# Kernel optimization log

Hardware: AMD Instinct MI355X
Metric: run time of the kernel (lower is better)

## Reference

```python
import jax, jax.numpy as jnp
import numpy as np

H = 512   # hidden_size == mm_dim
C = 8     # chunks
R = 8     # rank
S = H // C  # chunk size = 64
OUT = 512 # output_dim of linear_merge
EPS = 1e-12

def _linear(x, w, b):
    # torch nn.Linear convention: w [out, in]
    return x @ w.T + b

def setup_inputs() -> dict:
    key = jax.random.key(0)
    ks = jax.random.split(key, 24)
    B, Lq, Lk, D = 8, 160, 160, 512
    s = 0.02
    inp = {
        'v': jax.random.normal(ks[0], (B, Lk, D), jnp.float32),
        'k': jax.random.normal(ks[1], (B, Lk, D), jnp.float32),
        'q': jax.random.normal(ks[2], (B, Lq, D), jnp.float32),
        # input projections
        'w_v': jax.random.normal(ks[3], (H, D)) * s, 'b_v': jnp.zeros((H,)),
        'w_k': jax.random.normal(ks[4], (H, D)) * s, 'b_k': jnp.zeros((H,)),
        'w_q': jax.random.normal(ks[5], (H, D)) * s, 'b_q': jnp.zeros((H,)),
        # Block: linear0 (applied to key), linear1 (applied to query)
        'w0': jax.random.normal(ks[6], (H, H)) * s, 'b0': jnp.zeros((H,)),
        'w1': jax.random.normal(ks[7], (H, H)) * s, 'b1': jnp.zeros((H,)),
        # per-chunk merge linears, stacked: [C, S*R, S]
        'wm0': jax.random.normal(ks[8], (C, S * R, S)) * s, 'bm0': jnp.zeros((C, S * R)),
        'wm1': jax.random.normal(ks[9], (C, S * R, S)) * s, 'bm1': jnp.zeros((C, S * R)),
        # Block linear_out: mm_dim -> 1
        'w_bo': jax.random.normal(ks[10], (1, H)) * s, 'b_bo': jnp.zeros((1,)),
        # linear_merge: hidden -> output_dim
        'w_m': jax.random.normal(ks[11], (OUT, H)) * s, 'b_m': jnp.zeros((OUT,)),
    }
    return inp

def _block_scores(kx, qx, w0, b0, w1, b1, wm0, bm0, wm1, bm1, w_bo, b_bo):
    # kx: [B,Lk,H] (block arg 0 = key), qx: [B,Lq,H] (block arg 1 = query)
    x0 = _linear(kx, w0, b0)                      # [B,Lk,H]
    x1 = _linear(qx, w1, b1)                      # [B,Lq,H]
    B_, Lk = x0.shape[0], x0.shape[1]
    Lq = x1.shape[1]
    x0c = x0.reshape(B_, Lk, C, S)
    x1c = x1.reshape(B_, Lq, C, S)
    # per-chunk merge projections to rank*size
    y0 = jnp.einsum('bkcs,cts->bkct', x0c, wm0) + bm0  # [B,Lk,C,R*S]
    y1 = jnp.einsum('bqcs,cts->bqct', x1c, wm1) + bm1  # [B,Lq,C,R*S]
    y0 = y0.reshape(B_, Lk, C, R, S)
    y1 = y1.reshape(B_, Lq, C, R, S)
    # elementwise product summed over rank, pairwise over (q,k)
    z = jnp.einsum('bqcrs,bkcrs->bqkcs', y1, y0)  # [B,Lq,Lk,C,S]
    # signed sqrt (power norm) then per-chunk L2 normalize
    z = jnp.sqrt(jax.nn.relu(z)) - jnp.sqrt(jax.nn.relu(-z))
    z = z / jnp.maximum(jnp.linalg.norm(z, axis=-1, keepdims=True), EPS)
    z = z.reshape(B_, Lq, Lk, C * S)
    return _linear(z, w_bo, b_bo).squeeze(-1)     # [B,Lq,Lk]

def reference(v, k, q, w_v, b_v, w_k, b_k, w_q, b_q, w0, b0, w1, b1,
              wm0, bm0, wm1, bm1, w_bo, b_bo, w_m, b_m):
    vv = _linear(v, w_v, b_v)   # [B,Lk,H]
    kk = _linear(k, w_k, b_k)   # [B,Lk,H]
    qq = _linear(q, w_q, b_q)   # [B,Lq,H]
    scores = _block_scores(kk, qq, w0, b0, w1, b1, wm0, bm0, wm1, bm1, w_bo, b_bo)
    att = jax.nn.softmax(scores, axis=-1)          # dropout = identity (eval)
    atted = jnp.einsum('bqk,bkh->bqh', att, vv)    # [B,Lq,H]
    B_ = atted.shape[0]
    # faithful to torch: transpose(1,2).contiguous().view(B,-1,H)
    atted = jnp.swapaxes(atted, 1, 2).reshape(B_, -1, H)
    out = _linear(atted, w_m, b_m)                 # [B,Lq,OUT]
    return jnp.squeeze(out)
```

## Files before the change

kernel.cpp:

```cpp
#include <hip/hip_runtime.h>
#include <hip/hip_bf16.h>

#define B_  8
#define LQ  160
#define LK  160

typedef __attribute__((ext_vector_type(8))) short bf16x8;
typedef __attribute__((ext_vector_type(4))) float f32x4;

static __device__ __forceinline__ ushort f2bf(float f) {
    union { float f; unsigned u; } v; v.f = f;
    const unsigned r = (v.u + 0x7FFF + ((v.u >> 16) & 1)) >> 16;
    return (ushort)r;
}

struct CastArgs { const float4* src[6]; ushort4* dst[6]; int n[6]; };

__global__ __launch_bounds__(256) void cast_bf16k(CastArgs a)
{
    const int seg = blockIdx.y;
    const int i = blockIdx.x * 256 + threadIdx.x;
    if (i < a.n[seg]) {
        const float4 v = a.src[seg][i];
        ushort4 u;
        u.x = f2bf(v.x); u.y = f2bf(v.y); u.z = f2bf(v.z); u.w = f2bf(v.w);
        a.dst[seg][i] = u;
    }
}

struct MfmaOps { const ushort* A[2]; const ushort* W[2]; const float* Bi[2]; void* C[2]; };

template <int OUTBF>
__global__ __launch_bounds__(256) void mfma_g(MfmaOps ops)
{
    const int op = blockIdx.z;
    const ushort* __restrict__ A  = ops.A[op];
    const ushort* __restrict__ W  = ops.W[op];
    const float*  __restrict__ Bi = ops.Bi[op];

    const int m0 = blockIdx.y << 6;
    const int n0 = blockIdx.x << 6;
    const int tid  = threadIdx.x;
    const int wave = tid >> 6;
    const int lane = tid & 63;
    const int l16  = lane & 15;
    const int kg   = (lane >> 4) << 3;

    const ushort* Ap = A + (long)(m0 + (wave << 4) + l16) * 512 + kg;
    const ushort* Wp = W + (long)(n0 + l16) * 512 + kg;

    f32x4 acc[4] = {{0.f,0.f,0.f,0.f},{0.f,0.f,0.f,0.f},
                    {0.f,0.f,0.f,0.f},{0.f,0.f,0.f,0.f}};
    for (int k0 = 0; k0 < 512; k0 += 32) {
        const bf16x8 a = *(const bf16x8*)(Ap + k0);
#pragma unroll
        for (int nf = 0; nf < 4; nf++) {
            const bf16x8 b = *(const bf16x8*)(Wp + nf * (16 * 512) + k0);
            acc[nf] = __builtin_amdgcn_mfma_f32_16x16x32_bf16(a, b, acc[nf], 0, 0, 0);
        }
    }

    const int mrow = m0 + (wave << 4) + ((lane >> 4) << 2);
#pragma unroll
    for (int nf = 0; nf < 4; nf++) {
        const int n = n0 + (nf << 4) + l16;
        const float bias = Bi[n];
        if (OUTBF) {
            ushort* C = (ushort*)ops.C[op];
#pragma unroll
            for (int r = 0; r < 4; r++)
                C[(long)(mrow + r) * 512 + n] = f2bf(acc[nf][r] + bias);
        } else {
            float* C = (float*)ops.C[op];
#pragma unroll
            for (int r = 0; r < 4; r++)
                C[(long)(mrow + r) * 512 + n] = acc[nf][r] + bias;
        }
    }
}

struct GOps {
    const float* A[3];
    const float* W[3];
    const float* Bi[3];
    float*       C[3];
};

__global__ __launch_bounds__(256) void gemm_f(GOps ops, int K)
{
    const int op = blockIdx.z;
    const float* __restrict__ A  = ops.A[op];
    const float* __restrict__ W  = ops.W[op];
    const float* __restrict__ Bi = ops.Bi[op];
    float* __restrict__       C  = ops.C[op];

    const int m0 = blockIdx.y << 6;
    const int n0 = blockIdx.x << 6;
    const int tid = threadIdx.x;
    const int tm  = tid >> 4;
    const int tn  = tid & 15;
    const int lr  = tid >> 2;
    const int lk4 = (tid & 3) << 2;

    __shared__ float As[16][64];
    __shared__ float Ws[16][64];

    float acc[4][4];
#pragma unroll
    for (int i = 0; i < 4; i++)
#pragma unroll
        for (int j = 0; j < 4; j++) acc[i][j] = 0.f;

    const float* Arow = A + (long)(m0 + lr) * 512 + lk4;
    const float* Wrow = W + (long)(n0 + lr) * K + lk4;
    float4 av = *(const float4*)(Arow);
    float4 wv = *(const float4*)(Wrow);

    for (int k0 = 0; k0 < K; k0 += 16) {
        __syncthreads();
        As[lk4 + 0][lr] = av.x; As[lk4 + 1][lr] = av.y;
        As[lk4 + 2][lr] = av.z; As[lk4 + 3][lr] = av.w;
        Ws[lk4 + 0][lr] = wv.x; Ws[lk4 + 1][lr] = wv.y;
        Ws[lk4 + 2][lr] = wv.z; Ws[lk4 + 3][lr] = wv.w;
        __syncthreads();
        if (k0 + 16 < K) {
            av = *(const float4*)(Arow + k0 + 16);
            wv = *(const float4*)(Wrow + k0 + 16);
        }
#pragma unroll
        for (int kk = 0; kk < 16; kk++) {
            const float4 a4 = *(const float4*)(&As[kk][tm << 2]);
            const float4 b4 = *(const float4*)(&Ws[kk][tn << 2]);
            const float aa[4] = {a4.x, a4.y, a4.z, a4.w};
            const float bb[4] = {b4.x, b4.y, b4.z, b4.w};
#pragma unroll
            for (int i = 0; i < 4; i++)
#pragma unroll
                for (int j = 0; j < 4; j++)
                    acc[i][j] = fmaf(aa[i], bb[j], acc[i][j]);
        }
    }

    const float4 bv = *(const float4*)(Bi + n0 + (tn << 2));
    const float bArr[4] = {bv.x, bv.y, bv.z, bv.w};

#pragma unroll
    for (int i = 0; i < 4; i++) {
        float4 vo;
        vo.x = acc[i][0] + bArr[0]; vo.y = acc[i][1] + bArr[1];
        vo.z = acc[i][2] + bArr[2]; vo.w = acc[i][3] + bArr[3];
        *(float4*)(C + (long)(m0 + (tm << 2) + i) * 512 + n0 + (tn << 2)) = vo;
    }
}

__global__ __launch_bounds__(256) void y_proj(
    const float* __restrict__ x0, const float* __restrict__ wm0, const float* __restrict__ bm0,
    const float* __restrict__ x1, const float* __restrict__ wm1, const float* __restrict__ bm1,
    float* __restrict__ y0t, float* __restrict__ y1p)
{
    const int z   = blockIdx.z;
    const bool is1 = z >= 8;
    const int c   = is1 ? z - 8 : z;
    const float* A  = (is1 ? x1 : x0) + (c << 6);
    const float* W  = (is1 ? wm1 : wm0) + c * 32768;
    const float* Bi = (is1 ? bm1 : bm0) + (c << 9);

    const int m0 = blockIdx.y << 6;
    const int s0 = blockIdx.x << 3;
    const int tid = threadIdx.x;
    const int tm  = tid >> 4;
    const int tn  = tid & 15;
    const int lr  = tid >> 2;
    const int lk4 = (tid & 3) << 2;

    __shared__ float As[16][64];
    __shared__ float Ws[16][64];
    __shared__ float outT[4096];

    float acc[4][4];
#pragma unroll
    for (int i = 0; i < 4; i++)
#pragma unroll
        for (int j = 0; j < 4; j++) acc[i][j] = 0.f;

    const int wrow = ((lr & 7) << 6) + s0 + (lr >> 3);
    const float* Arow = A + (long)(m0 + lr) * 512 + lk4;
    const float* Wrow = W + (long)wrow * 64 + lk4;
    float4 av = *(const float4*)(Arow);
    float4 wv = *(const float4*)(Wrow);

    for (int k0 = 0; k0 < 64; k0 += 16) {
        __syncthreads();
        As[lk4 + 0][lr] = av.x; As[lk4 + 1][lr] = av.y;
        As[lk4 + 2][lr] = av.z; As[lk4 + 3][lr] = av.w;
        Ws[lk4 + 0][lr] = wv.x; Ws[lk4 + 1][lr] = wv.y;
        Ws[lk4 + 2][lr] = wv.z; Ws[lk4 + 3][lr] = wv.w;
        __syncthreads();
        if (k0 + 16 < 64) {
            av = *(const float4*)(Arow + k0 + 16);
            wv = *(const float4*)(Wrow + k0 + 16);
        }
#pragma unroll
        for (int kk = 0; kk < 16; kk++) {
            const float4 a4 = *(const float4*)(&As[kk][tm << 2]);
            const float4 b4 = *(const float4*)(&Ws[kk][tn << 2]);
            const float aa[4] = {a4.x, a4.y, a4.z, a4.w};
            const float bb[4] = {b4.x, b4.y, b4.z, b4.w};
#pragma unroll
            for (int i = 0; i < 4; i++)
#pragma unroll
                for (int j = 0; j < 4; j++)
                    acc[i][j] = fmaf(aa[i], bb[j], acc[i][j]);
        }
    }

    float bArr[4];
#pragma unroll
    for (int j = 0; j < 4; j++) {
        const int ln = (tn << 2) + j;
        bArr[j] = Bi[((ln & 7) << 6) + s0 + (ln >> 3)];
    }
    __syncthreads();
    if (is1) {
#pragma unroll
        for (int i = 0; i < 4; i++) {
            const int m8 = (tm << 2) + i;
#pragma unroll
            for (int j = 0; j < 4; j++) {
                const int ln = (tn << 2) + j;
                outT[(m8 << 6) + ((ln >> 3) << 3) + (ln & 7)] = acc[i][j] + bArr[j];
            }
        }
        __syncthreads();
#pragma unroll
        for (int p = 0; p < 4; p++) {
            const int idx = tid + (p << 8);
            const int m8  = idx >> 4;
            const int f4  = idx & 15;
            *(float4*)(y1p + (long)(m0 + m8) * 4096 + (c << 9) + (s0 << 3) + (f4 << 2))
                = *(const float4*)&outT[idx << 2];
        }
    } else {
#pragma unroll
        for (int i = 0; i < 4; i++) {
            const int k8 = (tm << 2) + i;
#pragma unroll
            for (int j = 0; j < 4; j++) {
                const int ln = (tn << 2) + j;
                outT[((ln >> 3) << 9) + (k8 << 3) + (ln & 7)] = acc[i][j] + bArr[j];
            }
        }
        __syncthreads();
#pragma unroll
        for (int p = 0; p < 4; p++) {
            const int s8  = (p << 1) + (tid >> 7);
            const int u4  = tid & 127;
            const int k8  = u4 >> 1;
            const int r   = (u4 & 1) << 2;
            const int m   = m0 + k8;
            const int bidx = m / 160;
            const int kmod = m - bidx * 160;
            const int s   = s0 + s8;
            float4* dst = (float4*)(y0t +
                (((long)(bidx * 8 + c) * 64 + s) * 160 + kmod) * 8 + r);
            *dst = *(const float4*)&outT[(s8 << 9) + (u4 << 2)];
        }
    }
}

__global__ __launch_bounds__(192) void score_partial(
    const float* __restrict__ y1p, const float* __restrict__ y0t,
    const float* __restrict__ wbo, float* __restrict__ scores_p)
{
    const int id = blockIdx.x;
    const int c  = id & 7;
    const int j  = id >> 3;
    const int b  = j / 40;
    const int q0 = (j - b * 40) << 2;
    const int k  = threadIdx.x;
    const int kc = k < LK ? k : (LK - 1);

    const float* wb = wbo + (c << 6);
    const float* y1r0 = y1p + (long)(b * LQ + q0) * 4096 + (c << 9);
    const float* y1r1 = y1r0 + 4096;
    const float* y1r2 = y1r0 + 8192;
    const float* y1r3 = y1r0 + 12288;
    const float* ybc = y0t + (((long)(b * 8 + c) * 64) * 160 + kc) * 8;

    float num[4] = {0.f, 0.f, 0.f, 0.f};
    float den[4] = {0.f, 0.f, 0.f, 0.f};

    float4 a0 = *(const float4*)(ybc);
    float4 a1 = *(const float4*)(ybc + 4);
#pragma unroll 2
    for (int s = 0; s < 64; s++) {
        const float a[8] = {a0.x, a0.y, a0.z, a0.w, a1.x, a1.y, a1.z, a1.w};
        const int sn = (s + 1) & 63;
        a0 = *(const float4*)(ybc + (long)sn * 1280);
        a1 = *(const float4*)(ybc + (long)sn * 1280 + 4);
        const float w = wb[s];
        const int o = s << 3;
        {
            float zv = a[0] * y1r0[o];
            zv = fmaf(a[1], y1r0[o+1], zv); zv = fmaf(a[2], y1r0[o+2], zv);
            zv = fmaf(a[3], y1r0[o+3], zv); zv = fmaf(a[4], y1r0[o+4], zv);
            zv = fmaf(a[5], y1r0[o+5], zv); zv = fmaf(a[6], y1r0[o+6], zv);
            zv = fmaf(a[7], y1r0[o+7], zv);
            const float az = fabsf(zv);
            num[0] = fmaf(copysignf(__builtin_amdgcn_sqrtf(az), zv), w, num[0]);
            den[0] += az;
        }
        {
            float zv = a[0] * y1r1[o];
            zv = fmaf(a[1], y1r1[o+1], zv); zv = fmaf(a[2], y1r1[o+2], zv);
            zv = fmaf(a[3], y1r1[o+3], zv); zv = fmaf(a[4], y1r1[o+4], zv);
            zv = fmaf(a[5], y1r1[o+5], zv); zv = fmaf(a[6], y1r1[o+6], zv);
            zv = fmaf(a[7], y1r1[o+7], zv);
            const float az = fabsf(zv);
            num[1] = fmaf(copysignf(__builtin_amdgcn_sqrtf(az), zv), w, num[1]);
            den[1] += az;
        }
        {
            float zv = a[0] * y1r2[o];
            zv = fmaf(a[1], y1r2[o+1], zv); zv = fmaf(a[2], y1r2[o+2], zv);
            zv = fmaf(a[3], y1r2[o+3], zv); zv = fmaf(a[4], y1r2[o+4], zv);
            zv = fmaf(a[5], y1r2[o+5], zv); zv = fmaf(a[6], y1r2[o+6], zv);
            zv = fmaf(a[7], y1r2[o+7], zv);
            const float az = fabsf(zv);
            num[2] = fmaf(copysignf(__builtin_amdgcn_sqrtf(az), zv), w, num[2]);
            den[2] += az;
        }
        {
            float zv = a[0] * y1r3[o];
            zv = fmaf(a[1], y1r3[o+1], zv); zv = fmaf(a[2], y1r3[o+2], zv);
            zv = fmaf(a[3], y1r3[o+3], zv); zv = fmaf(a[4], y1r3[o+4], zv);
            zv = fmaf(a[5], y1r3[o+5], zv); zv = fmaf(a[6], y1r3[o+6], zv);
            zv = fmaf(a[7], y1r3[o+7], zv);
            const float az = fabsf(zv);
            num[3] = fmaf(copysignf(__builtin_amdgcn_sqrtf(az), zv), w, num[3]);
            den[3] += az;
        }
    }
    if (k < LK) {
#pragma unroll
        for (int q = 0; q < 4; q++)
            scores_p[(((long)(b * LQ + q0 + q)) * 8 + c) * 160 + k] =
                num[q] / fmaxf(__builtin_amdgcn_sqrtf(den[q]), 1e-12f);
    }
}

__global__ __launch_bounds__(256) void softmax_attv(
    const float* __restrict__ scores_p, const float* __restrict__ vv,
    float* __restrict__ attedT)
{
    const int b  = blockIdx.y;
    const int q0 = blockIdx.x << 2;
    const int tid = threadIdx.x;

    __shared__ float scs[4][160];
    __shared__ float invd[4];

    for (int t = tid; t < 640; t += 256) {
        const int q = t / 160;
        const int k = t - q * 160;
        const float* sp = scores_p + ((long)(b * LQ + q0 + q)) * 1280 + k;
        float s = 0.f;
#pragma unroll
        for (int c = 0; c < 8; c++) s += sp[c * 160];
        scs[q][k] = s;
    }
    __syncthreads();

    const int w    = tid >> 6;
    const int lane = tid & 63;
    {
        const int q = w;
        float m = -1e30f;
        for (int kk = lane; kk < LK; kk += 64) m = fmaxf(m, scs[q][kk]);
#pragma unroll
        for (int off = 32; off; off >>= 1) m = fmaxf(m, __shfl_xor(m, off, 64));
        float sum = 0.f;
        for (int kk = lane; kk < LK; kk += 64) {
            const float e = __expf(scs[q][kk] - m);
            scs[q][kk] = e;
            sum += e;
        }
#pragma unroll
        for (int off = 32; off; off >>= 1) sum += __shfl_xor(sum, off, 64);
        if (lane == 0) invd[q] = 1.f / sum;
    }
    __syncthreads();

    float acc[2][4] = {{0.f,0.f,0.f,0.f},{0.f,0.f,0.f,0.f}};
    const float* vb = vv + (long)b * (LK * 512);
    for (int kk = 0; kk < LK; kk++) {
        const float* vr = vb + kk * 512;
        const float p0 = scs[0][kk], p1 = scs[1][kk];
        const float p2 = scs[2][kk], p3 = scs[3][kk];
        const float v0 = vr[tid], v1 = vr[tid + 256];
        acc[0][0] = fmaf(p0, v0, acc[0][0]); acc[0][1] = fmaf(p1, v0, acc[0][1]);
        acc[0][2] = fmaf(p2, v0, acc[0][2]); acc[0][3] = fmaf(p3, v0, acc[0][3]);
        acc[1][0] = fmaf(p0, v1, acc[1][0]); acc[1][1] = fmaf(p1, v1, acc[1][1]);
        acc[1][2] = fmaf(p2, v1, acc[1][2]); acc[1][3] = fmaf(p3, v1, acc[1][3]);
    }
#pragma unroll
    for (int j = 0; j < 2; j++) {
        const int h = tid + (j << 8);
#pragma unroll
        for (int q = 0; q < 4; q++)
            attedT[((long)b * 512 + h) * 160 + q0 + q] = acc[j][q] * invd[q];
    }
}

extern "C" void kernel_launch(void* const* d_in, const int* in_sizes, int n_in,
                              void* d_out, int out_size, void* d_ws, size_t ws_size,
                              hipStream_t stream) {
    const float* v    = (const float*)d_in[0];
    const float* kin  = (const float*)d_in[1];
    const float* q    = (const float*)d_in[2];
    const float* w_v  = (const float*)d_in[3];
    const float* b_v  = (const float*)d_in[4];
    const float* w_k  = (const float*)d_in[5];
    const float* b_k  = (const float*)d_in[6];
    const float* w_q  = (const float*)d_in[7];
    const float* b_q  = (const float*)d_in[8];
    const float* w0   = (const float*)d_in[9];
    const float* b0   = (const float*)d_in[10];
    const float* w1   = (const float*)d_in[11];
    const float* b1   = (const float*)d_in[12];
    const float* wm0  = (const float*)d_in[13];
    const float* bm0  = (const float*)d_in[14];
    const float* wm1  = (const float*)d_in[15];
    const float* bm1  = (const float*)d_in[16];
    const float* w_bo = (const float*)d_in[17];
    (void)d_in[18];
    const float* w_m  = (const float*)d_in[19];
    const float* b_m  = (const float*)d_in[20];

    float* ws       = (float*)d_ws;
    float* vv       = ws;
    ushort* kbf     = (ushort*)(ws + 655360);
    ushort* qbf     = kbf + 655360;
    ushort* kkbf    = (ushort*)(ws + 1310720);
    ushort* qqbf    = kkbf + 655360;
    float* x0       = ws + 1966080;
    float* x1       = ws + 2621440;
    float* y1p      = ws + 3276800;
    float* y0t      = ws + 8519680;
    float* attedT   = ws + 13762560;
    ushort* wkbf    = (ushort*)(ws + 14417920);
    ushort* wqbf    = wkbf + 262144;
    ushort* w0bf    = wkbf + 524288;
    ushort* w1bf    = wkbf + 786432;
    float* scores_p = ws + 655360;

    CastArgs ca;
    ca.src[0] = (const float4*)kin; ca.dst[0] = (ushort4*)kbf;  ca.n[0] = 163840;
    ca.src[1] = (const float4*)q;   ca.dst[1] = (ushort4*)qbf;  ca.n[1] = 163840;
    ca.src[2] = (const float4*)w_k; ca.dst[2] = (ushort4*)wkbf; ca.n[2] = 65536;
    ca.src[3] = (const float4*)w_q; ca.dst[3] = (ushort4*)wqbf; ca.n[3] = 65536;
    ca.src[4] = (const float4*)w0;  ca.dst[4] = (ushort4*)w0bf; ca.n[4] = 65536;
    ca.src[5] = (const float4*)w1;  ca.dst[5] = (ushort4*)w1bf; ca.n[5] = 65536;
    hipLaunchKernelGGL(cast_bf16k, dim3(640, 6), dim3(256), 0, stream, ca);

    GOps oV;
    oV.A[0] = v; oV.W[0] = w_v; oV.Bi[0] = b_v; oV.C[0] = vv;
    oV.A[1] = oV.A[2] = nullptr; oV.W[1] = oV.W[2] = nullptr;
    oV.Bi[1] = oV.Bi[2] = nullptr; oV.C[1] = oV.C[2] = nullptr;
    hipLaunchKernelGGL(gemm_f, dim3(8, 20, 1), dim3(256), 0, stream, oV, 512);

    MfmaOps mA;
    mA.A[0] = kbf; mA.W[0] = wkbf; mA.Bi[0] = b_k; mA.C[0] = kkbf;
    mA.A[1] = qbf; mA.W[1] = wqbf; mA.Bi[1] = b_q; mA.C[1] = qqbf;
    hipLaunchKernelGGL((mfma_g<1>), dim3(8, 20, 2), dim3(256), 0, stream, mA);

    MfmaOps mB;
    mB.A[0] = kkbf; mB.W[0] = w0bf; mB.Bi[0] = b0; mB.C[0] = x0;
    mB.A[1] = qqbf; mB.W[1] = w1bf; mB.Bi[1] = b1; mB.C[1] = x1;
    hipLaunchKernelGGL((mfma_g<0>), dim3(8, 20, 2), dim3(256), 0, stream, mB);

    hipLaunchKernelGGL(y_proj, dim3(8, 20, 16), dim3(256), 0, stream,
                       x0, wm0, bm0, x1, wm1, bm1, y0t, y1p);

    hipLaunchKernelGGL(score_partial, dim3(2560), dim3(192), 0, stream,
                       y1p, y0t, w_bo, scores_p);

    hipLaunchKernelGGL(softmax_attv, dim3(40, 8), dim3(256), 0, stream,
                       scores_p, vv, attedT);

    GOps oF;
    oF.A[0] = attedT; oF.W[0] = w_m; oF.Bi[0] = b_m; oF.C[0] = (float*)d_out;
    oF.A[1] = oF.A[2] = nullptr; oF.W[1] = oF.W[2] = nullptr;
    oF.Bi[1] = oF.Bi[2] = nullptr; oF.C[1] = oF.C[2] = nullptr;
    hipLaunchKernelGGL(gemm_f, dim3(8, 20, 1), dim3(256), 0, stream, oF, 512);
}
```

Before: 298.3 us.

## Compute pairwise rank-sum scores with bf16 MFMA and a shared y layout

y_proj now writes both y0 and y1 as bf16 in one common transposed layout [b,c,s,row,r]. The scalar FP32 score_partial kernel is replaced by score_mfma, which uses 16x16x32 bf16 MFMA to compute the rank-8 dot products for 16 queries by 32 keys per wave. Only 8 of the 32 K slots are filled and the rest are zeros. The aim is to cut the FP32 FMA work and halve the memory traffic of the y tensors, at the cost of bf16 rounding before the signed sqrt and a largely idle MFMA K dimension.

```diff
diff --git a/kernel.cpp b/kernel.cpp
--- a/kernel.cpp
+++ b/kernel.cpp
@@ -156,7 +156,7 @@
 __global__ __launch_bounds__(256) void y_proj(
     const float* __restrict__ x0, const float* __restrict__ wm0, const float* __restrict__ bm0,
     const float* __restrict__ x1, const float* __restrict__ wm1, const float* __restrict__ bm1,
-    float* __restrict__ y0t, float* __restrict__ y1p)
+    ushort* __restrict__ y0f, ushort* __restrict__ y1f)
 {
     const int z   = blockIdx.z;
     const bool is1 = z >= 8;
@@ -164,6 +164,7 @@
     const float* A  = (is1 ? x1 : x0) + (c << 6);
     const float* W  = (is1 ? wm1 : wm0) + c * 32768;
     const float* Bi = (is1 ? bm1 : bm0) + (c << 9);
+    ushort* __restrict__ dstT = is1 ? y1f : y0f;
 
     const int m0 = blockIdx.y << 6;
     const int s0 = blockIdx.x << 3;
@@ -221,131 +222,91 @@
         bArr[j] = Bi[((ln & 7) << 6) + s0 + (ln >> 3)];
     }
     __syncthreads();
-    if (is1) {
-#pragma unroll
-        for (int i = 0; i < 4; i++) {
-            const int m8 = (tm << 2) + i;
-#pragma unroll
-            for (int j = 0; j < 4; j++) {
-                const int ln = (tn << 2) + j;
-                outT[(m8 << 6) + ((ln >> 3) << 3) + (ln & 7)] = acc[i][j] + bArr[j];
-            }
-        }
-        __syncthreads();
-#pragma unroll
-        for (int p = 0; p < 4; p++) {
-            const int idx = tid + (p << 8);
-            const int m8  = idx >> 4;
-            const int f4  = idx & 15;
-            *(float4*)(y1p + (long)(m0 + m8) * 4096 + (c << 9) + (s0 << 3) + (f4 << 2))
-                = *(const float4*)&outT[idx << 2];
-        }
-    } else {
-#pragma unroll
-        for (int i = 0; i < 4; i++) {
-            const int k8 = (tm << 2) + i;
-#pragma unroll
-            for (int j = 0; j < 4; j++) {
-                const int ln = (tn << 2) + j;
-                outT[((ln >> 3) << 9) + (k8 << 3) + (ln & 7)] = acc[i][j] + bArr[j];
-            }
-        }
-        __syncthreads();
-#pragma unroll
-        for (int p = 0; p < 4; p++) {
-            const int s8  = (p << 1) + (tid >> 7);
-            const int u4  = tid & 127;
-            const int k8  = u4 >> 1;
-            const int r   = (u4 & 1) << 2;
-            const int m   = m0 + k8;
-            const int bidx = m / 160;
-            const int kmod = m - bidx * 160;
-            const int s   = s0 + s8;
-            float4* dst = (float4*)(y0t +
-                (((long)(bidx * 8 + c) * 64 + s) * 160 + kmod) * 8 + r);
-            *dst = *(const float4*)&outT[(s8 << 9) + (u4 << 2)];
-        }
-    }
-}
-
-__global__ __launch_bounds__(192) void score_partial(
-    const float* __restrict__ y1p, const float* __restrict__ y0t,
+#pragma unroll
+    for (int i = 0; i < 4; i++) {
+        const int r8 = (tm << 2) + i;
+#pragma unroll
+        for (int j = 0; j < 4; j++) {
+            const int ln = (tn << 2) + j;
+            outT[((ln >> 3) << 9) + (r8 << 3) + (ln & 7)] = acc[i][j] + bArr[j];
+        }
+    }
+    __syncthreads();
+#pragma unroll
+    for (int p = 0; p < 4; p++) {
+        const int s8  = (p << 1) + (tid >> 7);
+        const int u4  = tid & 127;
+        const int r8  = u4 >> 1;
+        const int r   = (u4 & 1) << 2;
+        const int m   = m0 + r8;
+        const int bidx = m / 160;
+        const int rmod = m - bidx * 160;
+        const int s   = s0 + s8;
+        const float* src = &outT[(s8 << 9) + (u4 << 2)];
+        ushort4 u;
+        u.x = f2bf(src[0]); u.y = f2bf(src[1]);
+        u.z = f2bf(src[2]); u.w = f2bf(src[3]);
+        *(ushort4*)(dstT + (((long)(bidx * 8 + c) * 64 + s) * 160 + rmod) * 8 + r) = u;
+    }
+}
+
+__global__ __launch_bounds__(320) void score_mfma(
+    const ushort* __restrict__ y1f, const ushort* __restrict__ y0f,
     const float* __restrict__ wbo, float* __restrict__ scores_p)
 {
-    const int id = blockIdx.x;
-    const int c  = id & 7;
-    const int j  = id >> 3;
-    const int b  = j / 40;
-    const int q0 = (j - b * 40) << 2;
-    const int k  = threadIdx.x;
-    const int kc = k < LK ? k : (LK - 1);
-
-    const float* wb = wbo + (c << 6);
-    const float* y1r0 = y1p + (long)(b * LQ + q0) * 4096 + (c << 9);
-    const float* y1r1 = y1r0 + 4096;
-    const float* y1r2 = y1r0 + 8192;
-    const float* y1r3 = y1r0 + 12288;
-    const float* ybc = y0t + (((long)(b * 8 + c) * 64) * 160 + kc) * 8;
-
-    float num[4] = {0.f, 0.f, 0.f, 0.f};
-    float den[4] = {0.f, 0.f, 0.f, 0.f};
-
-    float4 a0 = *(const float4*)(ybc);
-    float4 a1 = *(const float4*)(ybc + 4);
-#pragma unroll 2
+    const int bid = blockIdx.x;
+    const int c  = bid & 7;
+    const int b  = (bid >> 3) & 7;
+    const int qt = bid >> 6;
+    const int tid  = threadIdx.x;
+    const int wave = tid >> 6;
+    const int lane = tid & 63;
+    const int l16  = lane & 15;
+    const int g    = lane >> 4;
+    const int q0   = qt << 4;
+    const int k0   = wave << 5;
+
+    const long cbase = (long)(b * 8 + c) * 81920;
+    const float wreg = wbo[(c << 6) + lane];
+
+    f32x4 num0 = {0.f,0.f,0.f,0.f}, den0 = {0.f,0.f,0.f,0.f};
+    f32x4 num1 = {0.f,0.f,0.f,0.f}, den1 = {0.f,0.f,0.f,0.f};
+    const f32x4 zc = {0.f,0.f,0.f,0.f};
+    const bf16x8 zv8 = {0,0,0,0,0,0,0,0};
+
     for (int s = 0; s < 64; s++) {
-        const float a[8] = {a0.x, a0.y, a0.z, a0.w, a1.x, a1.y, a1.z, a1.w};
-        const int sn = (s + 1) & 63;
-        a0 = *(const float4*)(ybc + (long)sn * 1280);
-        a1 = *(const float4*)(ybc + (long)sn * 1280 + 4);
-        const float w = wb[s];
-        const int o = s << 3;
-        {
-            float zv = a[0] * y1r0[o];
-            zv = fmaf(a[1], y1r0[o+1], zv); zv = fmaf(a[2], y1r0[o+2], zv);
-            zv = fmaf(a[3], y1r0[o+3], zv); zv = fmaf(a[4], y1r0[o+4], zv);
-            zv = fmaf(a[5], y1r0[o+5], zv); zv = fmaf(a[6], y1r0[o+6], zv);
-            zv = fmaf(a[7], y1r0[o+7], zv);
-            const float az = fabsf(zv);
-            num[0] = fmaf(copysignf(__builtin_amdgcn_sqrtf(az), zv), w, num[0]);
-            den[0] += az;
-        }
-        {
-            float zv = a[0] * y1r1[o];
-            zv = fmaf(a[1], y1r1[o+1], zv); zv = fmaf(a[2], y1r1[o+2], zv);
-            zv = fmaf(a[3], y1r1[o+3], zv); zv = fmaf(a[4], y1r1[o+4], zv);
-            zv = fmaf(a[5], y1r1[o+5], zv); zv = fmaf(a[6], y1r1[o+6], zv);
-            zv = fmaf(a[7], y1r1[o+7], zv);
-            const float az = fabsf(zv);
-            num[1] = fmaf(copysignf(__builtin_amdgcn_sqrtf(az), zv), w, num[1]);
-            den[1] += az;
-        }
-        {
-            float zv = a[0] * y1r2[o];
-            zv = fmaf(a[1], y1r2[o+1], zv); zv = fmaf(a[2], y1r2[o+2], zv);
-            zv = fmaf(a[3], y1r2[o+3], zv); zv = fmaf(a[4], y1r2[o+4], zv);
-            zv = fmaf(a[5], y1r2[o+5], zv); zv = fmaf(a[6], y1r2[o+6], zv);
-            zv = fmaf(a[7], y1r2[o+7], zv);
-            const float az = fabsf(zv);
-            num[2] = fmaf(copysignf(__builtin_amdgcn_sqrtf(az), zv), w, num[2]);
-            den[2] += az;
-        }
-        {
-            float zv = a[0] * y1r3[o];
-            zv = fmaf(a[1], y1r3[o+1], zv); zv = fmaf(a[2], y1r3[o+2], zv);
-            zv = fmaf(a[3], y1r3[o+3], zv); zv = fmaf(a[4], y1r3[o+4], zv);
-            zv = fmaf(a[5], y1r3[o+5], zv); zv = fmaf(a[6], y1r3[o+6], zv);
-            zv = fmaf(a[7], y1r3[o+7], zv);
-            const float az = fabsf(zv);
-            num[3] = fmaf(copysignf(__builtin_amdgcn_sqrtf(az), zv), w, num[3]);
-            den[3] += az;
-        }
-    }
-    if (k < LK) {
-#pragma unroll
-        for (int q = 0; q < 4; q++)
-            scores_p[(((long)(b * LQ + q0 + q)) * 8 + c) * 160 + k] =
-                num[q] / fmaxf(__builtin_amdgcn_sqrtf(den[q]), 1e-12f);
+        const float w = __shfl(wreg, s, 64);
+        const ushort* row = y1f + cbase + (long)s * 1280;
+        const ushort* row0 = y0f + cbase + (long)s * 1280;
+        bf16x8 a = zv8, b0 = zv8, b1 = zv8;
+        if (g == 0) {
+            a  = *(const bf16x8*)(row  + (q0 + l16) * 8);
+            b0 = *(const bf16x8*)(row0 + (k0 + l16) * 8);
+            b1 = *(const bf16x8*)(row0 + (k0 + 16 + l16) * 8);
+        }
+        const f32x4 z0 = __builtin_amdgcn_mfma_f32_16x16x32_bf16(a, b0, zc, 0, 0, 0);
+        const f32x4 z1 = __builtin_amdgcn_mfma_f32_16x16x32_bf16(a, b1, zc, 0, 0, 0);
+#pragma unroll
+        for (int r4 = 0; r4 < 4; r4++) {
+            const float zz0 = z0[r4];
+            const float az0 = fabsf(zz0);
+            num0[r4] = fmaf(copysignf(__builtin_amdgcn_sqrtf(az0), zz0), w, num0[r4]);
+            den0[r4] += az0;
+            const float zz1 = z1[r4];
+            const float az1 = fabsf(zz1);
+            num1[r4] = fmaf(copysignf(__builtin_amdgcn_sqrtf(az1), zz1), w, num1[r4]);
+            den1[r4] += az1;
+        }
+    }
+
+#pragma unroll
+    for (int r4 = 0; r4 < 4; r4++) {
+        const int q = q0 + (g << 2) + r4;
+        const long rowb = ((long)(b * LQ + q) * 8 + c) * 160;
+        scores_p[rowb + k0 + l16] =
+            num0[r4] / fmaxf(__builtin_amdgcn_sqrtf(den0[r4]), 1e-12f);
+        scores_p[rowb + k0 + 16 + l16] =
+            num1[r4] / fmaxf(__builtin_amdgcn_sqrtf(den1[r4]), 1e-12f);
     }
 }
 
@@ -445,14 +406,14 @@
     ushort* qqbf    = kkbf + 655360;
     float* x0       = ws + 1966080;
     float* x1       = ws + 2621440;
-    float* y1p      = ws + 3276800;
-    float* y0t      = ws + 8519680;
-    float* attedT   = ws + 13762560;
-    ushort* wkbf    = (ushort*)(ws + 14417920);
+    ushort* y1f     = (ushort*)(ws + 3276800);
+    ushort* y0f     = (ushort*)(ws + 5898240);
+    float* attedT   = ws + 8519680;
+    float* scores_p = ws + 9175040;
+    ushort* wkbf    = (ushort*)(ws + 10813440);
     ushort* wqbf    = wkbf + 262144;
     ushort* w0bf    = wkbf + 524288;
     ushort* w1bf    = wkbf + 786432;
-    float* scores_p = ws + 655360;
 
     CastArgs ca;
     ca.src[0] = (const float4*)kin; ca.dst[0] = (ushort4*)kbf;  ca.n[0] = 163840;
@@ -480,10 +441,10 @@
     hipLaunchKernelGGL((mfma_g<0>), dim3(8, 20, 2), dim3(256), 0, stream, mB);
 
     hipLaunchKernelGGL(y_proj, dim3(8, 20, 16), dim3(256), 0, stream,
-                       x0, wm0, bm0, x1, wm1, bm1, y0t, y1p);
-
-    hipLaunchKernelGGL(score_partial, dim3(2560), dim3(192), 0, stream,
-                       y1p, y0t, w_bo, scores_p);
+                       x0, wm0, bm0, x1, wm1, bm1, y0f, y1f);
+
+    hipLaunchKernelGGL(score_mfma, dim3(640), dim3(320), 0, stream,
+                       y1f, y0f, w_bo, scores_p);
 
     hipLaunchKernelGGL(softmax_attv, dim3(40, 8), dim3(256), 0, stream,
                        scores_p, vv, attedT);
```

After: 260.5 us. -12.7%, faster.
